# Kernel optimization log

Measured on AMD Instinct MI355X. Metric: run time of the kernel, lower is better.

## Reference

```python
import jax, jax.numpy as jnp
import numpy as np

N_LAYERS = 4
N_WIRES = 10


def _apply_1q(state, U, wire, n):
    # state: [B, 2^n] complex64; U: [2,2] or [B,2,2]
    B = state.shape[0]
    a, b = 2 ** wire, 2 ** (n - wire - 1)
    s = state.reshape(B, a, 2, b)
    if U.ndim == 2:
        s = jnp.einsum('ij,bxjy->bxiy', U, s)
    else:
        s = jnp.einsum('bij,bxjy->bxiy', U, s)
    return s.reshape(B, -1)


def _apply_cnot(state, c, t, n):
    # CNOT with control c, target t (wire 0 = most significant bit, PennyLane convention)
    B = state.shape[0]
    q1, q2 = min(c, t), max(c, t)
    d1, d2, d3 = 2 ** q1, 2 ** (q2 - q1 - 1), 2 ** (n - q2 - 1)
    s = state.reshape(B, d1, 2, d2, 2, d3)
    if c < t:
        # control on axis 2, flip (X) target axis 4 where control bit == 1
        s = jnp.concatenate([s[:, :, 0:1], jnp.flip(s[:, :, 1:2], axis=4)], axis=2)
    else:
        # control on axis 4, flip target axis 2 where control bit == 1
        s = jnp.concatenate([s[:, :, :, :, 0:1], jnp.flip(s[:, :, :, :, 1:2], axis=2)], axis=4)
    return s.reshape(B, -1)


def _ry_mat(theta):
    # theta: [B] -> [B,2,2] complex64
    c, s = jnp.cos(theta / 2), jnp.sin(theta / 2)
    return jnp.stack([jnp.stack([c, -s], -1), jnp.stack([s, c], -1)], -2).astype(jnp.complex64)


def _rot_mat(phi, theta, omega):
    # qml.Rot(phi, theta, omega) = RZ(omega) @ RY(theta) @ RZ(phi)
    e = lambda a: jnp.exp(1j * a.astype(jnp.complex64))
    c = jnp.cos(theta / 2).astype(jnp.complex64)
    s = jnp.sin(theta / 2).astype(jnp.complex64)
    m00 = e(-0.5 * (phi + omega)) * c
    m01 = -e(0.5 * (phi - omega)) * s
    m10 = e(-0.5 * (phi - omega)) * s
    m11 = e(0.5 * (phi + omega)) * c
    return jnp.stack([jnp.stack([m00, m01]), jnp.stack([m10, m11])])


def setup_inputs() -> dict:
    key = jax.random.key(0)
    kx, kw = jax.random.split(key)
    X = jax.random.uniform(kx, (16384, N_WIRES), dtype=jnp.float32)
    # weightsStrongly = pi * U(0,1) of shape (n_layers, n_wires, 3)
    weights = np.pi * jax.random.uniform(kw, (N_LAYERS, N_WIRES, 3), dtype=jnp.float32)
    bias = jnp.zeros((1,), dtype=jnp.float32)
    return {"X": X, "weights": weights, "bias": bias}


def reference(X, weights, bias):
    B, n = X.shape
    L = weights.shape[0]
    # |0...0> batched statevector
    state = jnp.zeros((B, 2 ** n), dtype=jnp.complex64).at[:, 0].set(1.0)
    # angle encoding, gates='Y': RY(x_i * pi/2) on wire i (per-sample angle)
    for w in range(n):
        state = _apply_1q(state, _ry_mat(X[:, w] * (np.pi / 2)), w, n)
    # StronglyEntanglingLayers: Rot on each wire, then ring of CNOTs with range r_l
    for l in range(L):
        for w in range(n):
            U = _rot_mat(weights[l, w, 0], weights[l, w, 1], weights[l, w, 2])
            state = _apply_1q(state, U, w, n)
        r = l % (n - 1) + 1
        for w in range(n):
            state = _apply_cnot(state, w, (w + r) % n, n)
    # numClasses=2 -> single measurement: expval(PauliZ(wire n-1)) (last wire = LSB)
    probs = (state.real ** 2 + state.imag ** 2).reshape(B, 2 ** (n - 1), 2)
    z = jnp.sum(probs[..., 0] - probs[..., 1], axis=-1)  # [B]
    return z[:, None] + bias[None, :]  # [B, 1]
```

## Files before the change

### kernel.cpp

```cpp
#include <hip/hip_runtime.h>
#include <cstdint>
#include <utility>

#define NW 10
#define NL 4


struct Plan {
    int n;
    uint16_t pmask[40];
    uint16_t rmask[40];
    uint8_t  lw[40];
    uint16_t measmask;
};

constexpr bool keep_rot(int l, int w) {
    if (l <= 1) return true;
    if (l == 2) return w != 7;
    return w == 1 || w == 5 || w == 9;
}

constexpr Plan make_plan() {
    Plan P{};
    unsigned row[10], cI[10];
    for (int b = 0; b < 10; ++b) { row[b] = 1u << b; cI[b] = 1u << b; }
    P.n = 0;
    for (int l = 0; l < NL; ++l) {
        for (int w = 0; w < NW; ++w) {
            if (l > 0 && keep_rot(l, w)) {
                const int b = 9 - w;
                P.pmask[P.n] = (uint16_t)cI[b];
                P.rmask[P.n] = (uint16_t)row[b];
                P.lw[P.n]    = (uint8_t)(l * NW + w);
                P.n++;
            }
        }
        const int r = l % (NW - 1) + 1;
        for (int w = 0; w < NW; ++w) {
            const int cb = 9 - w, tb = 9 - ((w + r) % NW);
            row[tb] ^= row[cb];
            cI[cb]  ^= cI[tb];
        }
    }
    P.measmask = (uint16_t)row[0];
    return P;
}

constexpr Plan PL = make_plan();
constexpr int NROT = 22;
static_assert(PL.n == NROT, "plan size mismatch");

template<int MASK>
__device__ __forceinline__ float lane_xor(float v, int lane4 ) {
    if constexpr (MASK == 0) {
        return v;
    } else if constexpr (MASK < 32) {
        return __int_as_float(__builtin_amdgcn_ds_swizzle(
            __float_as_int(v), (MASK << 10) | 0x1F));
    } else {
        return __int_as_float(__builtin_amdgcn_ds_bpermute(
            lane4 ^ (MASK << 2), __float_as_int(v)));
    }
}

__device__ __forceinline__ void cmul(float ar, float ai, float br, float bi,
                                     float& cr, float& ci) {
    cr = ar * br - ai * bi;
    ci = ar * bi + ai * br;
}

template<int G>
__device__ __forceinline__ void apply_rot(float (&sr)[16], float (&si)[16],
                                          const float4* __restrict__ rotm,
                                          int lane, int lane4) {
    constexpr unsigned pm = PL.pmask[G], rm = PL.rmask[G];
    constexpr int pLoc = pm & 15, pLane = (int)(pm >> 4);
    constexpr int rLoc = rm & 15, rLane = (int)(rm >> 4);
    const float4 m = rotm[PL.lw[G]];
    const bool rl = (__popc(lane & rLane) & 1) != 0;
    const float cmr = m.x, coi = m.w;
    const float bmi = rl ? -m.y : m.y;
    const float bor = rl ? -m.z : m.z;

    if constexpr (pLane != 0) {
        if constexpr (pLoc == 0) {
#pragma unroll
            for (int j = 0; j < 16; ++j) {
                const float pr  = lane_xor<pLane>(sr[j], lane4);
                const float pi_ = lane_xor<pLane>(si[j], lane4);
                const float xr = sr[j], xi = si[j];
                if ((__builtin_popcount(j & rLoc) & 1) == 0) {
                    sr[j] = cmr*xr - bmi*xi + bor*pr - coi*pi_;
                    si[j] = cmr*xi + bmi*xr + bor*pi_ + coi*pr;
                } else {
                    sr[j] = cmr*xr + bmi*xi - bor*pr - coi*pi_;
                    si[j] = cmr*xi - bmi*xr - bor*pi_ + coi*pr;
                }
            }
        } else {
#pragma unroll
            for (int j = 0; j < 16; ++j) {
                const int k = j ^ pLoc;
                if (j < k) {
                    const float pjr = lane_xor<pLane>(sr[k], lane4);
                    const float pji = lane_xor<pLane>(si[k], lane4);
                    const float pkr = lane_xor<pLane>(sr[j], lane4);
                    const float pki = lane_xor<pLane>(si[j], lane4);
                    const float xjr = sr[j], xji = si[j];
                    const float xkr = sr[k], xki = si[k];
                    if ((__builtin_popcount(j & rLoc) & 1) == 0) {
                        sr[j] = cmr*xjr - bmi*xji + bor*pjr - coi*pji;
                        si[j] = cmr*xji + bmi*xjr + bor*pji + coi*pjr;
                    } else {
                        sr[j] = cmr*xjr + bmi*xji - bor*pjr - coi*pji;
                        si[j] = cmr*xji - bmi*xjr - bor*pji + coi*pjr;
                    }
                    if ((__builtin_popcount(k & rLoc) & 1) == 0) {
                        sr[k] = cmr*xkr - bmi*xki + bor*pkr - coi*pki;
                        si[k] = cmr*xki + bmi*xkr + bor*pki + coi*pkr;
                    } else {
                        sr[k] = cmr*xkr + bmi*xki - bor*pkr - coi*pki;
                        si[k] = cmr*xki - bmi*xkr - bor*pki + coi*pkr;
                    }
                }
            }
        }
    } else {
#pragma unroll
        for (int j = 0; j < 16; ++j) {
            const int k = j ^ pLoc;
            if (j < k) {
                const float xjr = sr[j], xji = si[j];
                const float xkr = sr[k], xki = si[k];
                if ((__builtin_popcount(j & rLoc) & 1) == 0) {
                    sr[j] = cmr*xjr - bmi*xji + bor*xkr - coi*xki;
                    si[j] = cmr*xji + bmi*xjr + bor*xki + coi*xkr;
                } else {
                    sr[j] = cmr*xjr + bmi*xji - bor*xkr - coi*xki;
                    si[j] = cmr*xji - bmi*xjr - bor*xki + coi*xkr;
                }
                if ((__builtin_popcount(k & rLoc) & 1) == 0) {
                    sr[k] = cmr*xkr - bmi*xki + bor*xjr - coi*xji;
                    si[k] = cmr*xki + bmi*xkr + bor*xji + coi*xjr;
                } else {
                    sr[k] = cmr*xkr + bmi*xki - bor*xjr - coi*xji;
                    si[k] = cmr*xki - bmi*xkr - bor*xji + coi*xjr;
                }
            }
        }
    }
}

template<int... Gs>
__device__ __forceinline__ void apply_all(float (&sr)[16], float (&si)[16],
                                          const float4* __restrict__ rotm,
                                          int lane, int lane4,
                                          std::integer_sequence<int, Gs...>) {
    (apply_rot<Gs>(sr, si, rotm, lane, lane4), ...);
}

__global__ __launch_bounds__(256) void vqc_kernel(const float* __restrict__ X,
                                                  const float* __restrict__ W,
                                                  const float* __restrict__ bias,
                                                  float* __restrict__ out,
                                                  int n_samples) {
    __shared__ float4 rotm[NL * NW];
    const int t = threadIdx.x;

    if (t < NL * NW) {
        const float phi = W[t * 3 + 0], th = W[t * 3 + 1], om = W[t * 3 + 2];
        float sh, ch; sincosf(0.5f * th, &sh, &ch);
        float s0, c0; sincosf(-0.5f * (phi + om), &s0, &c0);
        float s1, c1; sincosf( 0.5f * (phi - om), &s1, &c1);
        rotm[t] = make_float4(c0 * ch, s0 * ch, -c1 * sh, -s1 * sh);
    }
    __syncthreads();

    const int wave = (blockIdx.x * blockDim.x + t) >> 6;
    const int lane = t & 63;
    const int lane4 = lane << 2;
    if (wave >= n_samples) return;

    const float* xp = X + wave * NW;
    float v0r[NW], v0i[NW], v1r[NW], v1i[NW];
#pragma unroll
    for (int w = 0; w < NW; ++w) {
        float s, c;
        __sincosf(xp[w] * 0.78539816339744831f, &s, &c);
        const float4 m = rotm[w];
        v0r[w] =  m.x * c + m.z * s;
        v0i[w] =  m.y * c + m.w * s;
        v1r[w] = -m.z * c + m.x * s;
        v1i[w] =  m.w * c - m.y * s;
    }
    float hr, hi;
    {
        const bool b0 = (lane >> 5) & 1;
        hr = b0 ? v1r[0] : v0r[0];
        hi = b0 ? v1i[0] : v0i[0];
#pragma unroll
        for (int w = 1; w < 6; ++w) {
            const bool b = (lane >> (5 - w)) & 1;
            const float br = b ? v1r[w] : v0r[w];
            const float bi = b ? v1i[w] : v0i[w];
            float nr, ni; cmul(hr, hi, br, bi, nr, ni);
            hr = nr; hi = ni;
        }
    }
    float Ar[4], Ai[4], Br[4], Bi[4];
#pragma unroll
    for (int u = 0; u < 4; ++u) {
        const int hb = (u >> 1) & 1, lb = u & 1;
        cmul(hb ? v1r[6] : v0r[6], hb ? v1i[6] : v0i[6],
             lb ? v1r[7] : v0r[7], lb ? v1i[7] : v0i[7], Ar[u], Ai[u]);
        cmul(hb ? v1r[8] : v0r[8], hb ? v1i[8] : v0i[8],
             lb ? v1r[9] : v0r[9], lb ? v1i[9] : v0i[9], Br[u], Bi[u]);
    }
    float HAr[4], HAi[4];
#pragma unroll
    for (int u = 0; u < 4; ++u) cmul(hr, hi, Ar[u], Ai[u], HAr[u], HAi[u]);

    float sr[16], si[16];
#pragma unroll
    for (int j = 0; j < 16; ++j) {
        cmul(HAr[j >> 2], HAi[j >> 2], Br[j & 3], Bi[j & 3], sr[j], si[j]);
    }

    apply_all(sr, si, rotm, lane, lane4, std::make_integer_sequence<int, NROT>{});

    constexpr unsigned mm = PL.measmask;
    constexpr int mLoc = mm & 15, mLane = (int)(mm >> 4);
    float acc = 0.0f;
#pragma unroll
    for (int j = 0; j < 16; ++j) {
        const float p = sr[j] * sr[j] + si[j] * si[j];
        acc += ((__builtin_popcount(j & mLoc) & 1) ? -p : p);
    }
    if (__popc(lane & mLane) & 1) acc = -acc;
    acc += lane_xor<32>(acc, lane4);
    acc += lane_xor<16>(acc, lane4);
    acc += lane_xor<8>(acc, lane4);
    acc += lane_xor<4>(acc, lane4);
    acc += lane_xor<2>(acc, lane4);
    acc += lane_xor<1>(acc, lane4);
    if (lane == 0) out[wave] = acc + bias[0];
}

extern "C" void kernel_launch(void* const* d_in, const int* in_sizes, int n_in,
                              void* d_out, int out_size, void* d_ws, size_t ws_size,
                              hipStream_t stream) {
    const float* X    = (const float*)d_in[0];
    const float* W    = (const float*)d_in[1];
    const float* bias = (const float*)d_in[2];
    float* out = (float*)d_out;
    const int n_samples = in_sizes[0] / NW;
    const int threads = 256;
    const int blocks = (n_samples * 64 + threads - 1) / threads;
    hipLaunchKernelGGL(vqc_kernel, dim3(blocks), dim3(threads), 0, stream,
                       X, W, bias, out, n_samples);
}
```

Before: 131.8 us.

## Process two samples per wave with packed float2 math and DPP lane shuffles

Each wavefront now simulates two samples at once, holding the statevector as float2 vectors so the gate updates can lower to packed FP32 (v_pk_fma) instructions. This halves the number of waves and amortises the rotation-parameter loads and sign logic across two samples. Lane exchanges for masks 1, 2, 3, 7 and 15 now use DPP moves instead of ds_swizzle, avoiding LDS-path latency. Register pressure doubles, which may lower occupancy. An odd sample count would leave the last sample uncomputed.

After: 129.8 us. No clear change (-1.5%).

```diff
diff --git a/kernel.cpp b/kernel.cpp
--- a/kernel.cpp
+++ b/kernel.cpp
@@ -5,6 +5,8 @@
 #define NW 10
 #define NL 4
 
+
+typedef float v2 __attribute__((ext_vector_type(2)));
 
 struct Plan {
     int n;
@@ -51,9 +53,17 @@
 static_assert(PL.n == NROT, "plan size mismatch");
 
 template<int MASK>
-__device__ __forceinline__ float lane_xor(float v, int lane4 ) {
-    if constexpr (MASK == 0) {
-        return v;
+__device__ __forceinline__ float swz(float v, int lane4 ) {
+    if constexpr (MASK == 1) {
+        return __int_as_float(__builtin_amdgcn_mov_dpp(__float_as_int(v), 0xB1, 0xF, 0xF, true));
+    } else if constexpr (MASK == 2) {
+        return __int_as_float(__builtin_amdgcn_mov_dpp(__float_as_int(v), 0x4E, 0xF, 0xF, true));
+    } else if constexpr (MASK == 3) {
+        return __int_as_float(__builtin_amdgcn_mov_dpp(__float_as_int(v), 0x1B, 0xF, 0xF, true));
+    } else if constexpr (MASK == 7) {
+        return __int_as_float(__builtin_amdgcn_mov_dpp(__float_as_int(v), 0x141, 0xF, 0xF, true));
+    } else if constexpr (MASK == 15) {
+        return __int_as_float(__builtin_amdgcn_mov_dpp(__float_as_int(v), 0x140, 0xF, 0xF, true));
     } else if constexpr (MASK < 32) {
         return __int_as_float(__builtin_amdgcn_ds_swizzle(
             __float_as_int(v), (MASK << 10) | 0x1F));
@@ -63,14 +73,33 @@
     }
 }
 
-__device__ __forceinline__ void cmul(float ar, float ai, float br, float bi,
-                                     float& cr, float& ci) {
+template<int MASK>
+__device__ __forceinline__ v2 swz2(v2 v, int lane4) {
+    v2 r;
+    r.x = swz<MASK>(v.x, lane4);
+    r.y = swz<MASK>(v.y, lane4);
+    return r;
+}
+
+__device__ __forceinline__ v2 mkv2(float a, float b) { v2 r; r.x = a; r.y = b; return r; }
+
+__device__ __forceinline__ void cmul2(v2 ar, v2 ai, v2 br, v2 bi, v2& cr, v2& ci) {
     cr = ar * br - ai * bi;
     ci = ar * bi + ai * br;
 }
 
+__device__ __forceinline__ void upd(v2& xr, v2& xi, v2 pr, v2 pi,
+                                    float cmr, float coi, float bmi, float bor,
+                                    bool S) {
+    const float emi = S ? -bmi : bmi;
+    const float eor = S ? -bor : bor;
+    const v2 nr = cmr * xr - emi * xi + eor * pr - coi * pi;
+    const v2 ni = cmr * xi + emi * xr + eor * pi + coi * pr;
+    xr = nr; xi = ni;
+}
+
 template<int G>
-__device__ __forceinline__ void apply_rot(float (&sr)[16], float (&si)[16],
+__device__ __forceinline__ void apply_rot(v2 (&sr)[16], v2 (&si)[16],
                                           const float4* __restrict__ rotm,
                                           int lane, int lane4) {
     constexpr unsigned pm = PL.pmask[G], rm = PL.rmask[G];
@@ -82,77 +111,47 @@
     const float bmi = rl ? -m.y : m.y;
     const float bor = rl ? -m.z : m.z;
 
-    if constexpr (pLane != 0) {
-        if constexpr (pLoc == 0) {
-#pragma unroll
-            for (int j = 0; j < 16; ++j) {
-                const float pr  = lane_xor<pLane>(sr[j], lane4);
-                const float pi_ = lane_xor<pLane>(si[j], lane4);
-                const float xr = sr[j], xi = si[j];
-                if ((__builtin_popcount(j & rLoc) & 1) == 0) {
-                    sr[j] = cmr*xr - bmi*xi + bor*pr - coi*pi_;
-                    si[j] = cmr*xi + bmi*xr + bor*pi_ + coi*pr;
-                } else {
-                    sr[j] = cmr*xr + bmi*xi - bor*pr - coi*pi_;
-                    si[j] = cmr*xi - bmi*xr - bor*pi_ + coi*pr;
-                }
-            }
-        } else {
-#pragma unroll
-            for (int j = 0; j < 16; ++j) {
-                const int k = j ^ pLoc;
-                if (j < k) {
-                    const float pjr = lane_xor<pLane>(sr[k], lane4);
-                    const float pji = lane_xor<pLane>(si[k], lane4);
-                    const float pkr = lane_xor<pLane>(sr[j], lane4);
-                    const float pki = lane_xor<pLane>(si[j], lane4);
-                    const float xjr = sr[j], xji = si[j];
-                    const float xkr = sr[k], xki = si[k];
-                    if ((__builtin_popcount(j & rLoc) & 1) == 0) {
-                        sr[j] = cmr*xjr - bmi*xji + bor*pjr - coi*pji;
-                        si[j] = cmr*xji + bmi*xjr + bor*pji + coi*pjr;
-                    } else {
-                        sr[j] = cmr*xjr + bmi*xji - bor*pjr - coi*pji;
-                        si[j] = cmr*xji - bmi*xjr - bor*pji + coi*pjr;
-                    }
-                    if ((__builtin_popcount(k & rLoc) & 1) == 0) {
-                        sr[k] = cmr*xkr - bmi*xki + bor*pkr - coi*pki;
-                        si[k] = cmr*xki + bmi*xkr + bor*pki + coi*pkr;
-                    } else {
-                        sr[k] = cmr*xkr + bmi*xki - bor*pkr - coi*pki;
-                        si[k] = cmr*xki - bmi*xkr - bor*pki + coi*pkr;
-                    }
-                }
-            }
-        }
-    } else {
+    if constexpr (pLane == 0) {
 #pragma unroll
         for (int j = 0; j < 16; ++j) {
             const int k = j ^ pLoc;
             if (j < k) {
-                const float xjr = sr[j], xji = si[j];
-                const float xkr = sr[k], xki = si[k];
-                if ((__builtin_popcount(j & rLoc) & 1) == 0) {
-                    sr[j] = cmr*xjr - bmi*xji + bor*xkr - coi*xki;
-                    si[j] = cmr*xji + bmi*xjr + bor*xki + coi*xkr;
-                } else {
-                    sr[j] = cmr*xjr + bmi*xji - bor*xkr - coi*xki;
-                    si[j] = cmr*xji - bmi*xjr - bor*xki + coi*xkr;
-                }
-                if ((__builtin_popcount(k & rLoc) & 1) == 0) {
-                    sr[k] = cmr*xkr - bmi*xki + bor*xjr - coi*xji;
-                    si[k] = cmr*xki + bmi*xkr + bor*xji + coi*xjr;
-                } else {
-                    sr[k] = cmr*xkr + bmi*xki - bor*xjr - coi*xji;
-                    si[k] = cmr*xki - bmi*xkr - bor*xji + coi*xjr;
-                }
+                const v2 ajr = sr[j], aji = si[j];
+                const v2 akr = sr[k], aki = si[k];
+                upd(sr[j], si[j], akr, aki, cmr, coi, bmi, bor,
+                    (__builtin_popcount(j & rLoc) & 1) != 0);
+                upd(sr[k], si[k], ajr, aji, cmr, coi, bmi, bor,
+                    (__builtin_popcount(k & rLoc) & 1) != 0);
             }
         }
+    } else if constexpr (pLoc == 0) {
+#pragma unroll
+        for (int j = 0; j < 16; ++j) {
+            const v2 pr = swz2<pLane>(sr[j], lane4);
+            const v2 pi = swz2<pLane>(si[j], lane4);
+            upd(sr[j], si[j], pr, pi, cmr, coi, bmi, bor,
+                (__builtin_popcount(j & rLoc) & 1) != 0);
+        }
+    } else {
+#pragma unroll
+        for (int j = 0; j < 16; ++j) {
+            const int k = j ^ pLoc;
+            if (j < k) {
+                const v2 pjr = swz2<pLane>(sr[k], lane4);
+                const v2 pji = swz2<pLane>(si[k], lane4);
+                const v2 pkr = swz2<pLane>(sr[j], lane4);
+                const v2 pki = swz2<pLane>(si[j], lane4);
+                upd(sr[j], si[j], pjr, pji, cmr, coi, bmi, bor,
+                    (__builtin_popcount(j & rLoc) & 1) != 0);
+                upd(sr[k], si[k], pkr, pki, cmr, coi, bmi, bor,
+                    (__builtin_popcount(k & rLoc) & 1) != 0);
+            }
+        }
     }
 }
 
 template<int... Gs>
-__device__ __forceinline__ void apply_all(float (&sr)[16], float (&si)[16],
+__device__ __forceinline__ void apply_all(v2 (&sr)[16], v2 (&si)[16],
                                           const float4* __restrict__ rotm,
                                           int lane, int lane4,
                                           std::integer_sequence<int, Gs...>) {
@@ -163,7 +162,7 @@
                                                   const float* __restrict__ W,
                                                   const float* __restrict__ bias,
                                                   float* __restrict__ out,
-                                                  int n_samples) {
+                                                  int n_pairs) {
     __shared__ float4 rotm[NL * NW];
     const int t = threadIdx.x;
 
@@ -179,71 +178,85 @@
     const int wave = (blockIdx.x * blockDim.x + t) >> 6;
     const int lane = t & 63;
     const int lane4 = lane << 2;
-    if (wave >= n_samples) return;
-
-    const float* xp = X + wave * NW;
-    float v0r[NW], v0i[NW], v1r[NW], v1i[NW];
-#pragma unroll
-    for (int w = 0; w < NW; ++w) {
-        float s, c;
-        __sincosf(xp[w] * 0.78539816339744831f, &s, &c);
+    if (wave >= n_pairs) return;
+
+    const float* xp = X + (size_t)(2 * wave) * NW;
+
+    v2 hr, hi;
+#pragma unroll
+    for (int w = 0; w < 6; ++w) {
+        float s0, c0, s1, c1;
+        __sincosf(xp[w]      * 0.78539816339744831f, &s0, &c0);
+        __sincosf(xp[w + NW] * 0.78539816339744831f, &s1, &c1);
+        const v2 s = mkv2(s0, s1), c = mkv2(c0, c1);
         const float4 m = rotm[w];
-        v0r[w] =  m.x * c + m.z * s;
-        v0i[w] =  m.y * c + m.w * s;
-        v1r[w] = -m.z * c + m.x * s;
-        v1i[w] =  m.w * c - m.y * s;
-    }
-    float hr, hi;
-    {
-        const bool b0 = (lane >> 5) & 1;
-        hr = b0 ? v1r[0] : v0r[0];
-        hi = b0 ? v1i[0] : v0i[0];
-#pragma unroll
-        for (int w = 1; w < 6; ++w) {
-            const bool b = (lane >> (5 - w)) & 1;
-            const float br = b ? v1r[w] : v0r[w];
-            const float bi = b ? v1i[w] : v0i[w];
-            float nr, ni; cmul(hr, hi, br, bi, nr, ni);
+        const v2 a0r = m.x * c + m.z * s;
+        const v2 a0i = m.y * c + m.w * s;
+        const v2 a1r = m.x * s - m.z * c;
+        const v2 a1i = m.w * c - m.y * s;
+        const bool b = (lane >> (5 - w)) & 1;
+        const v2 br = b ? a1r : a0r;
+        const v2 bi = b ? a1i : a0i;
+        if (w == 0) { hr = br; hi = bi; }
+        else {
+            v2 nr, ni; cmul2(hr, hi, br, bi, nr, ni);
             hr = nr; hi = ni;
         }
     }
-    float Ar[4], Ai[4], Br[4], Bi[4];
+    v2 t0r[4], t0i[4], t1r[4], t1i[4];
+#pragma unroll
+    for (int w = 6; w < 10; ++w) {
+        float s0, c0, s1, c1;
+        __sincosf(xp[w]      * 0.78539816339744831f, &s0, &c0);
+        __sincosf(xp[w + NW] * 0.78539816339744831f, &s1, &c1);
+        const v2 s = mkv2(s0, s1), c = mkv2(c0, c1);
+        const float4 m = rotm[w];
+        t0r[w - 6] = m.x * c + m.z * s;
+        t0i[w - 6] = m.y * c + m.w * s;
+        t1r[w - 6] = m.x * s - m.z * c;
+        t1i[w - 6] = m.w * c - m.y * s;
+    }
+    v2 Ar[4], Ai[4], Br[4], Bi[4];
 #pragma unroll
     for (int u = 0; u < 4; ++u) {
         const int hb = (u >> 1) & 1, lb = u & 1;
-        cmul(hb ? v1r[6] : v0r[6], hb ? v1i[6] : v0i[6],
-             lb ? v1r[7] : v0r[7], lb ? v1i[7] : v0i[7], Ar[u], Ai[u]);
-        cmul(hb ? v1r[8] : v0r[8], hb ? v1i[8] : v0i[8],
-             lb ? v1r[9] : v0r[9], lb ? v1i[9] : v0i[9], Br[u], Bi[u]);
-    }
-    float HAr[4], HAi[4];
-#pragma unroll
-    for (int u = 0; u < 4; ++u) cmul(hr, hi, Ar[u], Ai[u], HAr[u], HAi[u]);
-
-    float sr[16], si[16];
+        cmul2(hb ? t1r[0] : t0r[0], hb ? t1i[0] : t0i[0],
+              lb ? t1r[1] : t0r[1], lb ? t1i[1] : t0i[1], Ar[u], Ai[u]);
+        cmul2(hb ? t1r[2] : t0r[2], hb ? t1i[2] : t0i[2],
+              lb ? t1r[3] : t0r[3], lb ? t1i[3] : t0i[3], Br[u], Bi[u]);
+    }
+    v2 HAr[4], HAi[4];
+#pragma unroll
+    for (int u = 0; u < 4; ++u) cmul2(hr, hi, Ar[u], Ai[u], HAr[u], HAi[u]);
+
+    v2 sr[16], si[16];
 #pragma unroll
     for (int j = 0; j < 16; ++j) {
-        cmul(HAr[j >> 2], HAi[j >> 2], Br[j & 3], Bi[j & 3], sr[j], si[j]);
+        cmul2(HAr[j >> 2], HAi[j >> 2], Br[j & 3], Bi[j & 3], sr[j], si[j]);
     }
 
     apply_all(sr, si, rotm, lane, lane4, std::make_integer_sequence<int, NROT>{});
 
     constexpr unsigned mm = PL.measmask;
     constexpr int mLoc = mm & 15, mLane = (int)(mm >> 4);
-    float acc = 0.0f;
+    v2 acc = mkv2(0.0f, 0.0f);
 #pragma unroll
     for (int j = 0; j < 16; ++j) {
-        const float p = sr[j] * sr[j] + si[j] * si[j];
-        acc += ((__builtin_popcount(j & mLoc) & 1) ? -p : p);
+        const v2 p = sr[j] * sr[j] + si[j] * si[j];
+        if (__builtin_popcount(j & mLoc) & 1) acc -= p; else acc += p;
     }
     if (__popc(lane & mLane) & 1) acc = -acc;
-    acc += lane_xor<32>(acc, lane4);
-    acc += lane_xor<16>(acc, lane4);
-    acc += lane_xor<8>(acc, lane4);
-    acc += lane_xor<4>(acc, lane4);
-    acc += lane_xor<2>(acc, lane4);
-    acc += lane_xor<1>(acc, lane4);
-    if (lane == 0) out[wave] = acc + bias[0];
+    acc += swz2<1>(acc, lane4);
+    acc += swz2<2>(acc, lane4);
+    acc += swz2<4>(acc, lane4);
+    acc += swz2<8>(acc, lane4);
+    acc += swz2<16>(acc, lane4);
+    acc += swz2<32>(acc, lane4);
+    if (lane == 0) {
+        const float b0 = bias[0];
+        out[2 * wave]     = acc.x + b0;
+        out[2 * wave + 1] = acc.y + b0;
+    }
 }
 
 extern "C" void kernel_launch(void* const* d_in, const int* in_sizes, int n_in,
@@ -254,8 +267,9 @@
     const float* bias = (const float*)d_in[2];
     float* out = (float*)d_out;
     const int n_samples = in_sizes[0] / NW;
+    const int n_pairs = n_samples / 2;
     const int threads = 256;
-    const int blocks = (n_samples * 64 + threads - 1) / threads;
+    const int blocks = (n_pairs * 64 + threads - 1) / threads;
     hipLaunchKernelGGL(vqc_kernel, dim3(blocks), dim3(threads), 0, stream,
-                       X, W, bias, out, n_samples);
-}
+                       X, W, bias, out, n_pairs);
+}
```
